# Kernel optimization log

Hardware: AMD Instinct MI355X
Metric: run time of the kernel (lower is better)

The kernel has to match this reference:

```python
import jax, jax.numpy as jnp
import numpy as np

N = 50000      # nodes
E = 800000     # edges (before self-loops)
DIN = 64
DH = 64
DOUT = 64
G = 500        # graphs in batch
EPS = 1e-5     # BatchNorm eps


def setup_inputs() -> dict:
    key = jax.random.key(0)
    ks = jax.random.split(key, 8)
    x = jax.random.normal(ks[0], (N, DIN), dtype=jnp.float32)
    edge_index = jax.random.randint(ks[1], (2, E), 0, N, dtype=jnp.int32)
    batch = jnp.sort(jax.random.randint(ks[2], (N,), 0, G, dtype=jnp.int32))

    def lin(k, di, do):
        return (jax.random.normal(k, (di, do), dtype=jnp.float32) / np.float32(np.sqrt(di)))

    inp = dict(x=x, edge_index=edge_index, batch=batch)
    dims = [(DIN, DH), (DH, DH), (DH, DOUT)]
    for i, (di, do) in enumerate(dims, start=1):
        inp[f"W{i}"] = lin(ks[2 + i], di, do)
        inp[f"b{i}"] = jnp.zeros((do,), jnp.float32)
        inp[f"gamma{i}"] = jnp.ones((do,), jnp.float32)
        inp[f"beta{i}"] = jnp.zeros((do,), jnp.float32)
    return inp


def _gcn_norm(edge_index, n_nodes):
    # add self loops, compute symmetric normalization deg^-1/2 * deg^-1/2
    loop = jnp.arange(n_nodes, dtype=edge_index.dtype)
    src = jnp.concatenate([edge_index[0], loop])
    dst = jnp.concatenate([edge_index[1], loop])
    deg = jax.ops.segment_sum(jnp.ones_like(dst, dtype=jnp.float32), dst,
                              num_segments=n_nodes)
    dinv = jax.lax.rsqrt(deg)  # deg >= 1 thanks to self-loops
    norm = dinv[src] * dinv[dst]  # [E + N]
    return src, dst, norm


def _gcn_conv(x, src, dst, norm, W, b, n_nodes):
    h = x @ W                               # [N, dout]
    msg = h[src] * norm[:, None]            # gather + scale  [E+N, dout]
    out = jax.ops.segment_sum(msg, dst, num_segments=n_nodes)  # scatter-add
    return out + b


def _batchnorm(x, gamma, beta):
    mean = jnp.mean(x, axis=0)
    var = jnp.mean(jnp.square(x - mean), axis=0)  # biased, as in torch training BN
    return gamma * (x - mean) * jax.lax.rsqrt(var + EPS) + beta


def reference(x, edge_index, batch, W1, b1, gamma1, beta1,
              W2, b2, gamma2, beta2, W3, b3, gamma3, beta3):
    src, dst, norm = _gcn_norm(edge_index, N)
    layers = [(W1, b1, gamma1, beta1), (W2, b2, gamma2, beta2),
              (W3, b3, gamma3, beta3)]
    h = x
    for i, (W, b, g, be) in enumerate(layers):
        h = _gcn_conv(h, src, dst, norm, W, b, N)
        h = _batchnorm(h, g, be)
        if i < len(layers) - 1:
            h = jax.nn.relu(h)  # dropout is identity in eval / reference
    # global mean pool over graphs
    sums = jax.ops.segment_sum(h, batch, num_segments=G)          # [G, DOUT]
    cnts = jax.ops.segment_sum(jnp.ones((N,), jnp.float32), batch,
                               num_segments=G)
    return sums / jnp.maximum(cnts, 1.0)[:, None]
```

## Files before the change

### kernel.cpp

```cpp
#include <hip/hip_runtime.h>

#define BN_EPS 1e-5f
#define CCH 4096
#define NSLICE 32


__device__ inline unsigned pack_bf16x2(float x, float y) {
    unsigned ux = __float_as_uint(x);
    ux = (ux + 0x7FFFu + ((ux >> 16) & 1u)) >> 16;
    unsigned uy = __float_as_uint(y);
    uy = (uy + 0x7FFFu + ((uy >> 16) & 1u)) >> 16;
    return ux | (uy << 16);
}

__device__ inline void bf16x2_add(unsigned u, float& a, float& b) {
    a += __uint_as_float((u & 0xFFFFu) << 16);
    b += __uint_as_float(u & 0xFFFF0000u);
}


__global__ __launch_bounds__(256) void coarse_count(const int* __restrict__ dst,
                                                    int* __restrict__ ccnt, int E) {
    __shared__ int h[256];
    int t = threadIdx.x;
    h[t] = 0;
    __syncthreads();
    int e0 = blockIdx.x * CCH;
#pragma unroll
    for (int k = 0; k < CCH / 256; ++k) {
        int e = e0 + k * 256 + t;
        if (e < E) atomicAdd(&h[dst[e] >> 8], 1);
    }
    __syncthreads();
    if (h[t]) atomicAdd(&ccnt[t], h[t]);
}

__global__ __launch_bounds__(256) void cscan(const int* __restrict__ ccnt,
                                             int* __restrict__ cboff,
                                             int* __restrict__ gcur,
                                             int* __restrict__ rp,
                                             float* __restrict__ cnt_g,
                                             float* __restrict__ out,
                                             int NBC, int n, int E, int G) {
    __shared__ int s[256];
    int t = threadIdx.x;
    int v = (t < NBC) ? ccnt[t] : 0;
    s[t] = v;
    __syncthreads();
    for (int off = 1; off < 256; off <<= 1) {
        int u = (t >= off) ? s[t - off] : 0;
        __syncthreads();
        s[t] += u;
        __syncthreads();
    }
    int ex = s[t] - v;
    if (t < NBC) { cboff[t] = ex; gcur[t] = ex; }
    if (t == 0) { cboff[NBC] = E; rp[n] = E; }
    for (int i = t; i < G; i += 256) cnt_g[i] = 0.f;
    int tot = G * 64;
    for (int i = t; i < tot; i += 256) out[i] = 0.f;
}

__global__ __launch_bounds__(256) void cscatter(const int* __restrict__ src,
                                                const int* __restrict__ dst,
                                                int* __restrict__ gcur,
                                                unsigned* __restrict__ tmp, int E) {
    __shared__ int lcnt[256];
    int t = threadIdx.x;
    int e0 = blockIdx.x * CCH;
    lcnt[t] = 0;
    __syncthreads();
#pragma unroll
    for (int k = 0; k < CCH / 256; ++k) {
        int e = e0 + k * 256 + t;
        if (e < E) atomicAdd(&lcnt[dst[e] >> 8], 1);
    }
    __syncthreads();
    int c = lcnt[t];
    __syncthreads();
    if (c > 0) lcnt[t] = atomicAdd(&gcur[t], c);
    __syncthreads();
#pragma unroll
    for (int k = 0; k < CCH / 256; ++k) {
        int e = e0 + k * 256 + t;
        if (e < E) {
            int d = dst[e];
            int pos = atomicAdd(&lcnt[d >> 8], 1);
            tmp[pos] = ((unsigned)src[e] << 8) | (unsigned)(d & 255);
        }
    }
}


#define OUT_CAP 8192

__global__ __launch_bounds__(256) void build_csr(const unsigned* __restrict__ tmp,
                                                 const int* __restrict__ cboff,
                                                 int* __restrict__ rp,
                                                 unsigned short* __restrict__ col,
                                                 float* __restrict__ dinv,
                                                 const int* __restrict__ batch,
                                                 float* __restrict__ cnt_g,
                                                 int n, int G) {
    __shared__ int hist[256];
    __shared__ int sc[256];
    __shared__ unsigned short outw[OUT_CAP];
    __shared__ int h[512];
    int b = blockIdx.x;
    int t = threadIdx.x;
    int beg = cboff[b], end = cboff[b + 1];
    int m = end - beg;
    hist[t] = 0;
    __syncthreads();
    for (int e = beg + t; e < end; e += 256) atomicAdd(&hist[tmp[e] & 255u], 1);
    __syncthreads();
    int v = hist[t];
    sc[t] = v;
    __syncthreads();
    for (int off = 1; off < 256; off <<= 1) {
        int u = (t >= off) ? sc[t - off] : 0;
        __syncthreads();
        sc[t] += u;
        __syncthreads();
    }
    int excl = sc[t] - v;
    int node = b * 256 + t;
    if (node < n) {
        dinv[node] = rsqrtf(1.0f + (float)v);
        rp[node] = beg + excl;
    }
    hist[t] = excl;
    __syncthreads();
    if (m <= OUT_CAP) {
        for (int e = beg + t; e < end; e += 256) {
            unsigned p = tmp[e];
            int pos = atomicAdd(&hist[p & 255u], 1);
            outw[pos] = (unsigned short)(p >> 8);
        }
        __syncthreads();
        for (int i = t; i < m; i += 256) col[beg + i] = outw[i];
    } else {
        for (int e = beg + t; e < end; e += 256) {
            unsigned p = tmp[e];
            int pos = atomicAdd(&hist[p & 255u], 1);
            col[beg + pos] = (unsigned short)(p >> 8);
        }
    }
    if (G <= 512) {
        __syncthreads();
        for (int i = t; i < 512; i += 256) h[i] = 0;
        __syncthreads();
        for (int i = b * 256 + t; i < n; i += gridDim.x * 256)
            atomicAdd(&h[batch[i]], 1);
        __syncthreads();
        for (int i = t; i < G; i += 256)
            if (h[i]) atomicAdd(&cnt_g[i], (float)h[i]);
    } else {
        for (int i = b * 256 + t; i < n; i += gridDim.x * 256)
            atomicAdd(&cnt_g[batch[i]], 1.0f);
    }
}


#define SXS 68

__global__ __launch_bounds__(256) void gemm64_v2(const float* __restrict__ X,
                                                 const float* __restrict__ W,
                                                 const float* __restrict__ dinv,
                                                 const float* __restrict__ part,
                                                 const float* __restrict__ gamma,
                                                 const float* __restrict__ beta,
                                                 int has_bn, float inv_n,
                                                 unsigned* __restrict__ Hs, int n) {
    __shared__ float sX[64 * SXS];
    __shared__ float sW[64 * SXS];
    __shared__ float s_scsh[128];
    int t = threadIdx.x;
    int c4 = t & 15;
    int base = blockIdx.x * 64;

    if (has_bn) {
        if (t < 128) {
            float s = 0.f;
#pragma unroll
            for (int k = 0; k < NSLICE; ++k) s += part[k * 128 + t];
            s_scsh[t] = s;
        }
        __syncthreads();
        if (t < 64) {
            float mean = s_scsh[t] * inv_n;
            float var = s_scsh[64 + t] * inv_n - mean * mean;
            float sc = gamma[t] * rsqrtf(var + BN_EPS);
            s_scsh[t] = sc;
            s_scsh[64 + t] = beta[t] - mean * sc;
        }
        __syncthreads();
    }

    {
        const float4* W4 = (const float4*)W;
#pragma unroll
        for (int it = 0; it < 4; ++it) {
            int idx = it * 256 + t;
            int r = idx >> 4;
            float4 v = W4[r * 16 + c4];
            *(float4*)&sW[r * SXS + c4 * 4] = v;
        }
    }
    {
        const float4* X4 = (const float4*)X;
        float4 sc4, sh4;
        if (has_bn) {
            sc4 = *(const float4*)&s_scsh[c4 * 4];
            sh4 = *(const float4*)&s_scsh[64 + c4 * 4];
        }
#pragma unroll
        for (int it = 0; it < 4; ++it) {
            int idx = it * 256 + t;
            int r = idx >> 4;
            int grow = base + r;
            float4 v = make_float4(0.f, 0.f, 0.f, 0.f);
            if (grow < n) v = X4[(size_t)grow * 16 + c4];
            if (has_bn) {
                v.x = fmaxf(fmaf(v.x, sc4.x, sh4.x), 0.f);
                v.y = fmaxf(fmaf(v.y, sc4.y, sh4.y), 0.f);
                v.z = fmaxf(fmaf(v.z, sc4.z, sh4.z), 0.f);
                v.w = fmaxf(fmaf(v.w, sc4.w, sh4.w), 0.f);
            }
            *(float4*)&sX[r * SXS + c4 * 4] = v;
        }
    }
    __syncthreads();

    int rgrp = t >> 4;
    float4 acc[4];
#pragma unroll
    for (int ri = 0; ri < 4; ++ri) acc[ri] = make_float4(0.f, 0.f, 0.f, 0.f);

#pragma unroll 4
    for (int k4 = 0; k4 < 16; ++k4) {
        float4 xv[4], wv[4];
#pragma unroll
        for (int ri = 0; ri < 4; ++ri)
            xv[ri] = *(const float4*)&sX[(rgrp + 16 * ri) * SXS + k4 * 4];
#pragma unroll
        for (int kk = 0; kk < 4; ++kk)
            wv[kk] = *(const float4*)&sW[(k4 * 4 + kk) * SXS + c4 * 4];
#pragma unroll
        for (int ri = 0; ri < 4; ++ri) {
            acc[ri].x = fmaf(xv[ri].x, wv[0].x, acc[ri].x);
            acc[ri].y = fmaf(xv[ri].x, wv[0].y, acc[ri].y);
            acc[ri].z = fmaf(xv[ri].x, wv[0].z, acc[ri].z);
            acc[ri].w = fmaf(xv[ri].x, wv[0].w, acc[ri].w);
            acc[ri].x = fmaf(xv[ri].y, wv[1].x, acc[ri].x);
            acc[ri].y = fmaf(xv[ri].y, wv[1].y, acc[ri].y);
            acc[ri].z = fmaf(xv[ri].y, wv[1].z, acc[ri].z);
            acc[ri].w = fmaf(xv[ri].y, wv[1].w, acc[ri].w);
            acc[ri].x = fmaf(xv[ri].z, wv[2].x, acc[ri].x);
            acc[ri].y = fmaf(xv[ri].z, wv[2].y, acc[ri].y);
            acc[ri].z = fmaf(xv[ri].z, wv[2].z, acc[ri].z);
            acc[ri].w = fmaf(xv[ri].z, wv[2].w, acc[ri].w);
            acc[ri].x = fmaf(xv[ri].w, wv[3].x, acc[ri].x);
            acc[ri].y = fmaf(xv[ri].w, wv[3].y, acc[ri].y);
            acc[ri].z = fmaf(xv[ri].w, wv[3].z, acc[ri].z);
            acc[ri].w = fmaf(xv[ri].w, wv[3].w, acc[ri].w);
        }
    }

#pragma unroll
    for (int ri = 0; ri < 4; ++ri) {
        int row = base + rgrp + 16 * ri;
        if (row < n) {
            float dv = dinv[row];
            uint2 o2;
            o2.x = pack_bf16x2(acc[ri].x * dv, acc[ri].y * dv);
            o2.y = pack_bf16x2(acc[ri].z * dv, acc[ri].w * dv);
            ((uint2*)Hs)[(size_t)row * 16 + c4] = o2;
        }
    }
}


__global__ __launch_bounds__(256) void agg(const uint2* __restrict__ Hs2,
                                           const int* __restrict__ rp,
                                           const unsigned short* __restrict__ col,
                                           const float* __restrict__ dinv,
                                           float* __restrict__ Y,
                                           float* __restrict__ part, int n) {
    __shared__ float sS[4][64];
    __shared__ float sQ[4][64];
    int t = threadIdx.x;
    int w = t >> 6;
    int lane = t & 63;
    int q = lane >> 4;
    int c = lane & 15;
    int d = blockIdx.x * 4 + w;
    bool valid = d < n;
    int dc = valid ? d : 0;
    float ax = 0.f, ay = 0.f, az = 0.f, aw = 0.f;
    int beg = valid ? rp[dc] : 0;
    int end = valid ? rp[dc + 1] : 0;
    for (int b = beg; b < end; b += 64) {
        int m = min(64, end - b);
        int myidx = (lane < m) ? (int)col[b + lane] : 0;
        int jj = 0;
        for (; jj + 7 < m; jj += 8) {
            int s0 = __shfl(myidx, jj + q, 64);
            int s1 = __shfl(myidx, jj + 4 + q, 64);
            uint2 v0 = Hs2[(size_t)s0 * 16 + c];
            uint2 v1 = Hs2[(size_t)s1 * 16 + c];
            bf16x2_add(v0.x, ax, ay); bf16x2_add(v0.y, az, aw);
            bf16x2_add(v1.x, ax, ay); bf16x2_add(v1.y, az, aw);
        }
        for (; jj < m; jj += 4) {
            int e = jj + q;
            int s0 = __shfl(myidx, min(e, m - 1), 64);
            if (e < m) {
                uint2 v = Hs2[(size_t)s0 * 16 + c];
                bf16x2_add(v.x, ax, ay); bf16x2_add(v.y, az, aw);
            }
        }
    }
    ax += __shfl_xor(ax, 16, 64); ay += __shfl_xor(ay, 16, 64);
    az += __shfl_xor(az, 16, 64); aw += __shfl_xor(aw, 16, 64);
    ax += __shfl_xor(ax, 32, 64); ay += __shfl_xor(ay, 32, 64);
    az += __shfl_xor(az, 32, 64); aw += __shfl_xor(aw, 32, 64);
    if (q == 0) {
        float4 y = make_float4(0.f, 0.f, 0.f, 0.f);
        if (valid) {
            float hx = 0.f, hy = 0.f, hz = 0.f, hw = 0.f;
            uint2 hv = Hs2[(size_t)dc * 16 + c];
            bf16x2_add(hv.x, hx, hy); bf16x2_add(hv.y, hz, hw);
            float dv = dinv[dc];
            y.x = (ax + hx) * dv; y.y = (ay + hy) * dv;
            y.z = (az + hz) * dv; y.w = (aw + hw) * dv;
            *(float4*)&Y[(size_t)dc * 64 + c * 4] = y;
        }
        *(float4*)&sS[w][c * 4] = y;
        float4 yq = make_float4(y.x * y.x, y.y * y.y, y.z * y.z, y.w * y.w);
        *(float4*)&sQ[w][c * 4] = yq;
    }
    __syncthreads();
    if (t < 64) {
        float s = sS[0][t] + sS[1][t] + sS[2][t] + sS[3][t];
        float qq = sQ[0][t] + sQ[1][t] + sQ[2][t] + sQ[3][t];
        float* dst = part + (size_t)(blockIdx.x & (NSLICE - 1)) * 128;
        atomicAdd(&dst[t], s);
        atomicAdd(&dst[64 + t], qq);
    }
}

__global__ __launch_bounds__(256) void agg_pool(const uint2* __restrict__ Hs2,
                                                const int* __restrict__ rp,
                                                const unsigned short* __restrict__ col,
                                                const float* __restrict__ dinv,
                                                const int* __restrict__ batch,
                                                float* __restrict__ out,
                                                float* __restrict__ part, int n) {
    __shared__ float sS[4][64];
    __shared__ float sQ[4][64];
    __shared__ int sG[4];
    int t = threadIdx.x;
    int w = t >> 6;
    int lane = t & 63;
    int q = lane >> 4;
    int c = lane & 15;
    int d = blockIdx.x * 4 + w;
    bool valid = d < n;
    int dc = valid ? d : 0;
    float ax = 0.f, ay = 0.f, az = 0.f, aw = 0.f;
    int beg = valid ? rp[dc] : 0;
    int end = valid ? rp[dc + 1] : 0;
    for (int b = beg; b < end; b += 64) {
        int m = min(64, end - b);
        int myidx = (lane < m) ? (int)col[b + lane] : 0;
        int jj = 0;
        for (; jj + 7 < m; jj += 8) {
            int s0 = __shfl(myidx, jj + q, 64);
            int s1 = __shfl(myidx, jj + 4 + q, 64);
            uint2 v0 = Hs2[(size_t)s0 * 16 + c];
            uint2 v1 = Hs2[(size_t)s1 * 16 + c];
            bf16x2_add(v0.x, ax, ay); bf16x2_add(v0.y, az, aw);
            bf16x2_add(v1.x, ax, ay); bf16x2_add(v1.y, az, aw);
        }
        for (; jj < m; jj += 4) {
            int e = jj + q;
            int s0 = __shfl(myidx, min(e, m - 1), 64);
            if (e < m) {
                uint2 v = Hs2[(size_t)s0 * 16 + c];
                bf16x2_add(v.x, ax, ay); bf16x2_add(v.y, az, aw);
            }
        }
    }
    ax += __shfl_xor(ax, 16, 64); ay += __shfl_xor(ay, 16, 64);
    az += __shfl_xor(az, 16, 64); aw += __shfl_xor(aw, 16, 64);
    ax += __shfl_xor(ax, 32, 64); ay += __shfl_xor(ay, 32, 64);
    az += __shfl_xor(az, 32, 64); aw += __shfl_xor(aw, 32, 64);
    if (q == 0) {
        float4 y = make_float4(0.f, 0.f, 0.f, 0.f);
        if (valid) {
            float hx = 0.f, hy = 0.f, hz = 0.f, hw = 0.f;
            uint2 hv = Hs2[(size_t)dc * 16 + c];
            bf16x2_add(hv.x, hx, hy); bf16x2_add(hv.y, hz, hw);
            float dv = dinv[dc];
            y.x = (ax + hx) * dv; y.y = (ay + hy) * dv;
            y.z = (az + hz) * dv; y.w = (aw + hw) * dv;
        }
        *(float4*)&sS[w][c * 4] = y;
        float4 yq = make_float4(y.x * y.x, y.y * y.y, y.z * y.z, y.w * y.w);
        *(float4*)&sQ[w][c * 4] = yq;
        if (lane == 0) sG[w] = valid ? batch[dc] : -1;
    }
    __syncthreads();
    if (t < 64) {
        float s = sS[0][t] + sS[1][t] + sS[2][t] + sS[3][t];
        float qq = sQ[0][t] + sQ[1][t] + sQ[2][t] + sQ[3][t];
        float* dst = part + (size_t)(blockIdx.x & (NSLICE - 1)) * 128;
        atomicAdd(&dst[t], s);
        atomicAdd(&dst[64 + t], qq);
        int g0 = sG[0], g1 = sG[1], g2 = sG[2], g3 = sG[3];
        if (g0 >= 0 && g0 == g1 && g0 == g2 && g0 == g3) {
            atomicAdd(&out[(size_t)g0 * 64 + t], s);
        } else {
            if (g0 >= 0) atomicAdd(&out[(size_t)g0 * 64 + t], sS[0][t]);
            if (g1 >= 0) atomicAdd(&out[(size_t)g1 * 64 + t], sS[1][t]);
            if (g2 >= 0) atomicAdd(&out[(size_t)g2 * 64 + t], sS[2][t]);
            if (g3 >= 0) atomicAdd(&out[(size_t)g3 * 64 + t], sS[3][t]);
        }
    }
}


__global__ __launch_bounds__(256) void pool_div(float* __restrict__ out,
                                                const float* __restrict__ cnt,
                                                const float* __restrict__ part,
                                                const float* __restrict__ gamma,
                                                const float* __restrict__ beta,
                                                int G, float inv_n) {
    __shared__ float s_scsh[128];
    int t = threadIdx.x;
    if (t < 128) {
        float s = 0.f;
#pragma unroll
        for (int k = 0; k < NSLICE; ++k) s += part[k * 128 + t];
        s_scsh[t] = s;
    }
    __syncthreads();
    if (t < 64) {
        float mean = s_scsh[t] * inv_n;
        float var = s_scsh[64 + t] * inv_n - mean * mean;
        float sc = gamma[t] * rsqrtf(var + BN_EPS);
        s_scsh[t] = sc;
        s_scsh[64 + t] = beta[t] - mean * sc;
    }
    __syncthreads();
    int idx = blockIdx.x * 256 + t;
    if (idx >= G * 64) return;
    int j = idx & 63, g = idx >> 6;
    float c = cnt[g];
    out[idx] = (c > 0.5f) ? fmaf(s_scsh[j], out[idx] / c, s_scsh[64 + j]) : 0.f;
}


extern "C" void kernel_launch(void* const* d_in, const int* in_sizes, int n_in,
                              void* d_out, int out_size, void* d_ws, size_t ws_size,
                              hipStream_t stream) {
    const float* x     = (const float*)d_in[0];
    const int*   ei    = (const int*)d_in[1];
    const int*   batch = (const int*)d_in[2];
    const float* Wl[3] = {(const float*)d_in[3], (const float*)d_in[7], (const float*)d_in[11]};
    const float* gl[3] = {(const float*)d_in[5], (const float*)d_in[9], (const float*)d_in[13]};
    const float* bl[3] = {(const float*)d_in[6], (const float*)d_in[10], (const float*)d_in[14]};
    float* out = (float*)d_out;

    int E = in_sizes[1] / 2;
    int n = in_sizes[0] / 64;
    int G = out_size / 64;
    const int* src = ei;
    const int* dst = ei + E;
    int NBC = (n + 255) / 256;
    float inv_n = 1.0f / (float)n;

    char* ws = (char*)d_ws;
    size_t off = 0;
    auto carve = [&](size_t bytes) {
        void* p = ws + off;
        off += (bytes + 255) & ~(size_t)255;
        return p;
    };
    float*          part  = (float*)carve(3 * NSLICE * 128 * 4);
    int*            ccnt  = (int*)carve(256 * 4);
    float*          dinv  = (float*)carve((size_t)n * 4);
    float*          cnt_g = (float*)carve((size_t)G * 4);
    unsigned*       Hs    = (unsigned*)carve((size_t)n * 32 * 4);
    float*          Ybuf  = (float*)carve((size_t)n * 64 * 4);
    int*            cboff = (int*)carve(257 * 4);
    int*            gcur  = (int*)carve(256 * 4);
    int*            rp    = (int*)carve(((size_t)n + 1) * 4);
    unsigned*       tmp   = (unsigned*)carve((size_t)E * 4);
    unsigned short* col   = (unsigned short*)carve((size_t)E * 2);

    int pgrid = (E + CCH - 1) / CCH;

    hipMemsetAsync(part, 0, 3 * NSLICE * 128 * 4 + 256 * 4, stream);
    coarse_count<<<pgrid, 256, 0, stream>>>(dst, ccnt, E);
    cscan<<<1, 256, 0, stream>>>(ccnt, cboff, gcur, rp, cnt_g, out, NBC, n, E, G);
    cscatter<<<pgrid, 256, 0, stream>>>(src, dst, gcur, tmp, E);
    build_csr<<<NBC, 256, 0, stream>>>(tmp, cboff, rp, col, dinv, batch, cnt_g, n, G);

    int gemm_grid = (n + 63) / 64;
    int agg_grid = (n + 3) / 4;

    const float* cur = x;
    for (int l = 0; l < 3; ++l) {
        float* part_l = part + (size_t)l * NSLICE * 128;
        const float* part_prev = (l > 0) ? part + (size_t)(l - 1) * NSLICE * 128 : part;
        gemm64_v2<<<gemm_grid, 256, 0, stream>>>(cur, Wl[l], dinv, part_prev,
                                                 l > 0 ? gl[l - 1] : gl[0],
                                                 l > 0 ? bl[l - 1] : bl[0],
                                                 l > 0 ? 1 : 0, inv_n, Hs, n);
        if (l < 2) {
            agg<<<agg_grid, 256, 0, stream>>>((const uint2*)Hs, rp, col, dinv,
                                              Ybuf, part_l, n);
        } else {
            agg_pool<<<agg_grid, 256, 0, stream>>>((const uint2*)Hs, rp, col, dinv,
                                                   batch, out, part_l, n);
        }
        cur = Ybuf;
    }

    pool_div<<<(G * 64 + 255) / 256, 256, 0, stream>>>(out, cnt_g,
                                                       part + 2 * NSLICE * 128,
                                                       gl[2], bl[2], G, inv_n);
}
```

Baseline: 255.8 us.

## Switch gathered features to fp16 with half2 accumulation and 16-byte loads

Stores the scaled GEMM output as fp16 instead of bf16, and the aggregation kernels now accumulate neighbor rows with packed half2 adds. Each lane loads 8 channels (uint4) instead of 4, so 8 neighbors are gathered in parallel per wave instead of 4. The aim is to cut the per-element unpack and FP32 add instructions and to issue wider, fewer memory requests in the gather-bound aggregation. The risk is fp16 accumulation over many neighbors: reduced precision and possible overflow compared with fp32 accumulation.

Result: no change. 253.8 us (-0.8%).

```diff
diff --git a/kernel.cpp b/kernel.cpp
--- a/kernel.cpp
+++ b/kernel.cpp
@@ -1,21 +1,20 @@
 #include <hip/hip_runtime.h>
+#include <hip/hip_fp16.h>
 
 #define BN_EPS 1e-5f
 #define CCH 4096
 #define NSLICE 32
 
 
-__device__ inline unsigned pack_bf16x2(float x, float y) {
-    unsigned ux = __float_as_uint(x);
-    ux = (ux + 0x7FFFu + ((ux >> 16) & 1u)) >> 16;
-    unsigned uy = __float_as_uint(y);
-    uy = (uy + 0x7FFFu + ((uy >> 16) & 1u)) >> 16;
-    return ux | (uy << 16);
-}
-
-__device__ inline void bf16x2_add(unsigned u, float& a, float& b) {
-    a += __uint_as_float((u & 0xFFFFu) << 16);
-    b += __uint_as_float(u & 0xFFFF0000u);
+__device__ inline __half2 u2h(unsigned u) {
+    union { unsigned u; __half2 h; } x; x.u = u; return x.h;
+}
+__device__ inline unsigned h2u(__half2 h) {
+    union { unsigned u; __half2 h; } x; x.h = h; return x.u;
+}
+
+__device__ inline unsigned pack_f16x2(float a, float b) {
+    return h2u(__floats2half2_rn(a, b));
 }
 
 
@@ -273,15 +272,15 @@
         if (row < n) {
             float dv = dinv[row];
             uint2 o2;
-            o2.x = pack_bf16x2(acc[ri].x * dv, acc[ri].y * dv);
-            o2.y = pack_bf16x2(acc[ri].z * dv, acc[ri].w * dv);
+            o2.x = pack_f16x2(acc[ri].x * dv, acc[ri].y * dv);
+            o2.y = pack_f16x2(acc[ri].z * dv, acc[ri].w * dv);
             ((uint2*)Hs)[(size_t)row * 16 + c4] = o2;
         }
     }
 }
 
 
-__global__ __launch_bounds__(256) void agg(const uint2* __restrict__ Hs2,
+__global__ __launch_bounds__(256) void agg(const uint4* __restrict__ Hs4,
                                            const int* __restrict__ rp,
                                            const unsigned short* __restrict__ col,
                                            const float* __restrict__ dinv,
@@ -292,53 +291,68 @@
     int t = threadIdx.x;
     int w = t >> 6;
     int lane = t & 63;
-    int q = lane >> 4;
-    int c = lane & 15;
+    int g = lane >> 3;
+    int c = lane & 7;
     int d = blockIdx.x * 4 + w;
     bool valid = d < n;
     int dc = valid ? d : 0;
-    float ax = 0.f, ay = 0.f, az = 0.f, aw = 0.f;
+    __half2 a0 = u2h(0u), a1 = u2h(0u), a2 = u2h(0u), a3 = u2h(0u);
     int beg = valid ? rp[dc] : 0;
     int end = valid ? rp[dc + 1] : 0;
     for (int b = beg; b < end; b += 64) {
         int m = min(64, end - b);
         int myidx = (lane < m) ? (int)col[b + lane] : 0;
         int jj = 0;
-        for (; jj + 7 < m; jj += 8) {
-            int s0 = __shfl(myidx, jj + q, 64);
-            int s1 = __shfl(myidx, jj + 4 + q, 64);
-            uint2 v0 = Hs2[(size_t)s0 * 16 + c];
-            uint2 v1 = Hs2[(size_t)s1 * 16 + c];
-            bf16x2_add(v0.x, ax, ay); bf16x2_add(v0.y, az, aw);
-            bf16x2_add(v1.x, ax, ay); bf16x2_add(v1.y, az, aw);
-        }
-        for (; jj < m; jj += 4) {
-            int e = jj + q;
-            int s0 = __shfl(myidx, min(e, m - 1), 64);
+        for (; jj + 15 < m; jj += 16) {
+            int s0 = __shfl(myidx, jj + g, 64);
+            int s1 = __shfl(myidx, jj + 8 + g, 64);
+            uint4 v0 = Hs4[(size_t)s0 * 8 + c];
+            uint4 v1 = Hs4[(size_t)s1 * 8 + c];
+            a0 = __hadd2(a0, u2h(v0.x)); a1 = __hadd2(a1, u2h(v0.y));
+            a2 = __hadd2(a2, u2h(v0.z)); a3 = __hadd2(a3, u2h(v0.w));
+            a0 = __hadd2(a0, u2h(v1.x)); a1 = __hadd2(a1, u2h(v1.y));
+            a2 = __hadd2(a2, u2h(v1.z)); a3 = __hadd2(a3, u2h(v1.w));
+        }
+        for (; jj < m; jj += 8) {
+            int e = jj + g;
+            int s0 = __shfl(myidx, e, 64);
             if (e < m) {
-                uint2 v = Hs2[(size_t)s0 * 16 + c];
-                bf16x2_add(v.x, ax, ay); bf16x2_add(v.y, az, aw);
+                uint4 v = Hs4[(size_t)s0 * 8 + c];
+                a0 = __hadd2(a0, u2h(v.x)); a1 = __hadd2(a1, u2h(v.y));
+                a2 = __hadd2(a2, u2h(v.z)); a3 = __hadd2(a3, u2h(v.w));
             }
         }
     }
-    ax += __shfl_xor(ax, 16, 64); ay += __shfl_xor(ay, 16, 64);
-    az += __shfl_xor(az, 16, 64); aw += __shfl_xor(aw, 16, 64);
-    ax += __shfl_xor(ax, 32, 64); ay += __shfl_xor(ay, 32, 64);
-    az += __shfl_xor(az, 32, 64); aw += __shfl_xor(aw, 32, 64);
-    if (q == 0) {
-        float4 y = make_float4(0.f, 0.f, 0.f, 0.f);
+#pragma unroll
+    for (int mask = 8; mask <= 32; mask <<= 1) {
+        a0 = __hadd2(a0, u2h((unsigned)__shfl_xor((int)h2u(a0), mask, 64)));
+        a1 = __hadd2(a1, u2h((unsigned)__shfl_xor((int)h2u(a1), mask, 64)));
+        a2 = __hadd2(a2, u2h((unsigned)__shfl_xor((int)h2u(a2), mask, 64)));
+        a3 = __hadd2(a3, u2h((unsigned)__shfl_xor((int)h2u(a3), mask, 64)));
+    }
+    if (g == 0) {
+        float2 f0 = __half22float2(a0), f1 = __half22float2(a1);
+        float2 f2 = __half22float2(a2), f3 = __half22float2(a3);
+        float y0 = f0.x, y1 = f0.y, y2 = f1.x, y3 = f1.y;
+        float y4 = f2.x, y5 = f2.y, y6 = f3.x, y7 = f3.y;
         if (valid) {
-            float hx = 0.f, hy = 0.f, hz = 0.f, hw = 0.f;
-            uint2 hv = Hs2[(size_t)dc * 16 + c];
-            bf16x2_add(hv.x, hx, hy); bf16x2_add(hv.y, hz, hw);
+            uint4 hv = Hs4[(size_t)dc * 8 + c];
+            float2 h0 = __half22float2(u2h(hv.x)), h1 = __half22float2(u2h(hv.y));
+            float2 h2v = __half22float2(u2h(hv.z)), h3 = __half22float2(u2h(hv.w));
             float dv = dinv[dc];
-            y.x = (ax + hx) * dv; y.y = (ay + hy) * dv;
-            y.z = (az + hz) * dv; y.w = (aw + hw) * dv;
-            *(float4*)&Y[(size_t)dc * 64 + c * 4] = y;
-        }
-        *(float4*)&sS[w][c * 4] = y;
-        float4 yq = make_float4(y.x * y.x, y.y * y.y, y.z * y.z, y.w * y.w);
-        *(float4*)&sQ[w][c * 4] = yq;
+            y0 = (y0 + h0.x) * dv; y1 = (y1 + h0.y) * dv;
+            y2 = (y2 + h1.x) * dv; y3 = (y3 + h1.y) * dv;
+            y4 = (y4 + h2v.x) * dv; y5 = (y5 + h2v.y) * dv;
+            y6 = (y6 + h3.x) * dv; y7 = (y7 + h3.y) * dv;
+            *(float4*)&Y[(size_t)dc * 64 + c * 8]     = make_float4(y0, y1, y2, y3);
+            *(float4*)&Y[(size_t)dc * 64 + c * 8 + 4] = make_float4(y4, y5, y6, y7);
+        } else {
+            y0 = y1 = y2 = y3 = y4 = y5 = y6 = y7 = 0.f;
+        }
+        *(float4*)&sS[w][c * 8]     = make_float4(y0, y1, y2, y3);
+        *(float4*)&sS[w][c * 8 + 4] = make_float4(y4, y5, y6, y7);
+        *(float4*)&sQ[w][c * 8]     = make_float4(y0 * y0, y1 * y1, y2 * y2, y3 * y3);
+        *(float4*)&sQ[w][c * 8 + 4] = make_float4(y4 * y4, y5 * y5, y6 * y6, y7 * y7);
     }
     __syncthreads();
     if (t < 64) {
@@ -350,7 +364,7 @@
     }
 }
 
-__global__ __launch_bounds__(256) void agg_pool(const uint2* __restrict__ Hs2,
+__global__ __launch_bounds__(256) void agg_pool(const uint4* __restrict__ Hs4,
                                                 const int* __restrict__ rp,
                                                 const unsigned short* __restrict__ col,
                                                 const float* __restrict__ dinv,
@@ -363,52 +377,66 @@
     int t = threadIdx.x;
     int w = t >> 6;
     int lane = t & 63;
-    int q = lane >> 4;
-    int c = lane & 15;
+    int g = lane >> 3;
+    int c = lane & 7;
     int d = blockIdx.x * 4 + w;
     bool valid = d < n;
     int dc = valid ? d : 0;
-    float ax = 0.f, ay = 0.f, az = 0.f, aw = 0.f;
+    __half2 a0 = u2h(0u), a1 = u2h(0u), a2 = u2h(0u), a3 = u2h(0u);
     int beg = valid ? rp[dc] : 0;
     int end = valid ? rp[dc + 1] : 0;
     for (int b = beg; b < end; b += 64) {
         int m = min(64, end - b);
         int myidx = (lane < m) ? (int)col[b + lane] : 0;
         int jj = 0;
-        for (; jj + 7 < m; jj += 8) {
-            int s0 = __shfl(myidx, jj + q, 64);
-            int s1 = __shfl(myidx, jj + 4 + q, 64);
-            uint2 v0 = Hs2[(size_t)s0 * 16 + c];
-            uint2 v1 = Hs2[(size_t)s1 * 16 + c];
-            bf16x2_add(v0.x, ax, ay); bf16x2_add(v0.y, az, aw);
-            bf16x2_add(v1.x, ax, ay); bf16x2_add(v1.y, az, aw);
-        }
-        for (; jj < m; jj += 4) {
-            int e = jj + q;
-            int s0 = __shfl(myidx, min(e, m - 1), 64);
+        for (; jj + 15 < m; jj += 16) {
+            int s0 = __shfl(myidx, jj + g, 64);
+            int s1 = __shfl(myidx, jj + 8 + g, 64);
+            uint4 v0 = Hs4[(size_t)s0 * 8 + c];
+            uint4 v1 = Hs4[(size_t)s1 * 8 + c];
+            a0 = __hadd2(a0, u2h(v0.x)); a1 = __hadd2(a1, u2h(v0.y));
+            a2 = __hadd2(a2, u2h(v0.z)); a3 = __hadd2(a3, u2h(v0.w));
+            a0 = __hadd2(a0, u2h(v1.x)); a1 = __hadd2(a1, u2h(v1.y));
+            a2 = __hadd2(a2, u2h(v1.z)); a3 = __hadd2(a3, u2h(v1.w));
+        }
+        for (; jj < m; jj += 8) {
+            int e = jj + g;
+            int s0 = __shfl(myidx, e, 64);
             if (e < m) {
-                uint2 v = Hs2[(size_t)s0 * 16 + c];
-                bf16x2_add(v.x, ax, ay); bf16x2_add(v.y, az, aw);
+                uint4 v = Hs4[(size_t)s0 * 8 + c];
+                a0 = __hadd2(a0, u2h(v.x)); a1 = __hadd2(a1, u2h(v.y));
+                a2 = __hadd2(a2, u2h(v.z)); a3 = __hadd2(a3, u2h(v.w));
             }
         }
     }
-    ax += __shfl_xor(ax, 16, 64); ay += __shfl_xor(ay, 16, 64);
-    az += __shfl_xor(az, 16, 64); aw += __shfl_xor(aw, 16, 64);
-    ax += __shfl_xor(ax, 32, 64); ay += __shfl_xor(ay, 32, 64);
-    az += __shfl_xor(az, 32, 64); aw += __shfl_xor(aw, 32, 64);
-    if (q == 0) {
-        float4 y = make_float4(0.f, 0.f, 0.f, 0.f);
+#pragma unroll
+    for (int mask = 8; mask <= 32; mask <<= 1) {
+        a0 = __hadd2(a0, u2h((unsigned)__shfl_xor((int)h2u(a0), mask, 64)));
+        a1 = __hadd2(a1, u2h((unsigned)__shfl_xor((int)h2u(a1), mask, 64)));
+        a2 = __hadd2(a2, u2h((unsigned)__shfl_xor((int)h2u(a2), mask, 64)));
+        a3 = __hadd2(a3, u2h((unsigned)__shfl_xor((int)h2u(a3), mask, 64)));
+    }
+    if (g == 0) {
+        float2 f0 = __half22float2(a0), f1 = __half22float2(a1);
+        float2 f2 = __half22float2(a2), f3 = __half22float2(a3);
+        float y0 = f0.x, y1 = f0.y, y2 = f1.x, y3 = f1.y;
+        float y4 = f2.x, y5 = f2.y, y6 = f3.x, y7 = f3.y;
         if (valid) {
-            float hx = 0.f, hy = 0.f, hz = 0.f, hw = 0.f;
-            uint2 hv = Hs2[(size_t)dc * 16 + c];
-            bf16x2_add(hv.x, hx, hy); bf16x2_add(hv.y, hz, hw);
+            uint4 hv = Hs4[(size_t)dc * 8 + c];
+            float2 h0 = __half22float2(u2h(hv.x)), h1 = __half22float2(u2h(hv.y));
+            float2 h2v = __half22float2(u2h(hv.z)), h3 = __half22float2(u2h(hv.w));
             float dv = dinv[dc];
-            y.x = (ax + hx) * dv; y.y = (ay + hy) * dv;
-            y.z = (az + hz) * dv; y.w = (aw + hw) * dv;
-        }
-        *(float4*)&sS[w][c * 4] = y;
-        float4 yq = make_float4(y.x * y.x, y.y * y.y, y.z * y.z, y.w * y.w);
-        *(float4*)&sQ[w][c * 4] = yq;
+            y0 = (y0 + h0.x) * dv; y1 = (y1 + h0.y) * dv;
+            y2 = (y2 + h1.x) * dv; y3 = (y3 + h1.y) * dv;
+            y4 = (y4 + h2v.x) * dv; y5 = (y5 + h2v.y) * dv;
+            y6 = (y6 + h3.x) * dv; y7 = (y7 + h3.y) * dv;
+        } else {
+            y0 = y1 = y2 = y3 = y4 = y5 = y6 = y7 = 0.f;
+        }
+        *(float4*)&sS[w][c * 8]     = make_float4(y0, y1, y2, y3);
+        *(float4*)&sS[w][c * 8 + 4] = make_float4(y4, y5, y6, y7);
+        *(float4*)&sQ[w][c * 8]     = make_float4(y0 * y0, y1 * y1, y2 * y2, y3 * y3);
+        *(float4*)&sQ[w][c * 8 + 4] = make_float4(y4 * y4, y5 * y5, y6 * y6, y7 * y7);
         if (lane == 0) sG[w] = valid ? batch[dc] : -1;
     }
     __syncthreads();
@@ -520,10 +548,10 @@
                                                  l > 0 ? bl[l - 1] : bl[0],
                                                  l > 0 ? 1 : 0, inv_n, Hs, n);
         if (l < 2) {
-            agg<<<agg_grid, 256, 0, stream>>>((const uint2*)Hs, rp, col, dinv,
+            agg<<<agg_grid, 256, 0, stream>>>((const uint4*)Hs, rp, col, dinv,
                                               Ybuf, part_l, n);
         } else {
-            agg_pool<<<agg_grid, 256, 0, stream>>>((const uint2*)Hs, rp, col, dinv,
+            agg_pool<<<agg_grid, 256, 0, stream>>>((const uint4*)Hs, rp, col, dinv,
                                                    batch, out, part_l, n);
         }
         cur = Ybuf;
```
